# Performance work log

Measured on AMD Instinct MI355X. Metric: run time of the kernel, lower is better.

Reference implementation:

```python
import jax, jax.numpy as jnp
import numpy as np

NUM_GROUPS = 32
EPS = 1e-5


def _conv(x, w, b, pad):
    # x: [B,C,H,W], w: [O,I,kh,kw]
    y = jax.lax.conv_general_dilated(
        x, w, window_strides=(1, 1), padding=[(pad, pad), (pad, pad)],
        dimension_numbers=('NCHW', 'OIHW', 'NCHW'))
    return y + b[None, :, None, None]


def _group_norm(x, gamma, beta):
    B, C, H, W = x.shape
    g = x.reshape(B, NUM_GROUPS, C // NUM_GROUPS, H, W)
    mu = g.mean(axis=(2, 3, 4), keepdims=True)
    var = g.var(axis=(2, 3, 4), keepdims=True)
    g = (g - mu) * jax.lax.rsqrt(var + EPS)
    x = g.reshape(B, C, H, W)
    return x * gamma[None, :, None, None] + beta[None, :, None, None]


def setup_inputs() -> dict:
    key = jax.random.key(0)
    ks = jax.random.split(key, 8)
    B, C, H, W = 8, 384, 64, 64
    s1 = 1.0 / np.sqrt(C)          # 1x1 conv fan-in
    s3 = 1.0 / np.sqrt(C * 9)      # 3x3 conv fan-in
    return {
        'x': jax.random.normal(ks[0], (B, C, H, W), dtype=jnp.float32),
        'gamma': jnp.ones((C,), dtype=jnp.float32),
        'beta': jnp.zeros((C,), dtype=jnp.float32),
        'wq': jax.random.normal(ks[1], (C, C, 1, 1), dtype=jnp.float32) * s1,
        'bq': jnp.zeros((C,), dtype=jnp.float32),
        'wk': jax.random.normal(ks[2], (C, C, 3, 3), dtype=jnp.float32) * s3,
        'bk': jnp.zeros((C,), dtype=jnp.float32),
        'wv': jax.random.normal(ks[3], (C, C, 1, 1), dtype=jnp.float32) * s1,
        'bv': jnp.zeros((C,), dtype=jnp.float32),
        'wf': jax.random.normal(ks[4], (C, C, 1, 1), dtype=jnp.float32) * s1,
        'bf': jnp.zeros((C,), dtype=jnp.float32),
        'k': 512,
    }


def reference(x, gamma, beta, wq, bq, wk, bk, wv, bv, wf, bf, k):
    B, C, H, W = x.shape
    xn = _group_norm(x, gamma, beta)
    q = _conv(xn, wq, bq, 0)
    kk = _conv(xn, wk, bk, 1)
    v = _conv(xn, wv, bv, 0)
    # frequency-domain correlation: elementwise product of 2D spectra
    Fq = jnp.fft.fft2(q)
    Fk = jnp.fft.fft2(kk)
    A = jnp.fft.ifft2(Fq * Fk).real          # [B,C,H,W]
    # per-(batch,channel) spatial top-k sparsification
    A_flat = A.reshape(B, C, H * W)
    topv, _ = jax.lax.top_k(A_flat, k)
    thresh = topv[..., -1:]                   # k-th largest value
    masked = jnp.where(A_flat >= thresh, A_flat, -jnp.inf)
    Fw = jax.nn.softmax(masked, axis=-1).reshape(B, C, H, W)
    F4 = v * Fw                               # weighted values
    res = _conv(F4, wf, bf, 0)
    return xn * res
```

## Files before the change

kernel.cpp:

```cpp
#include <hip/hip_runtime.h>
#include <hip/hip_fp16.h>
#include <math.h>

#define CCH  384
#define BATCH 8
#define HWN  4096
#define NG   32
#define CPG  12
#define KSEL 512
#define FFTP 65

typedef short v8s  __attribute__((ext_vector_type(8)));
typedef float v16f __attribute__((ext_vector_type(16)));

#define MFMA_B16(A_,B_,C_) __builtin_amdgcn_mfma_f32_32x32x16_bf16((A_),(B_),(C_),0,0,0)

#define BARRIER_RAW() asm volatile("s_barrier" ::: "memory")

__device__ __forceinline__ void gl16(const unsigned short* g, unsigned short* l) {
  __builtin_amdgcn_global_load_lds(
      (const __attribute__((address_space(1))) unsigned int*)g,
      (__attribute__((address_space(3))) unsigned int*)l, 16, 0, 0);
}

__device__ __forceinline__ v8s as_v8s(uint4 u) {
  union { uint4 u4; v8s v; } c; c.u4 = u; return c.v;
}
__device__ __forceinline__ unsigned br6(unsigned i) {
  return ((i&1u)<<5)|((i&2u)<<3)|((i&4u)<<1)|((i&8u)>>1)|((i&16u)>>3)|((i&32u)>>5);
}
__device__ __forceinline__ unsigned f2key(float f) {
  unsigned u = __float_as_uint(f);
  return (u & 0x80000000u) ? ~u : (u | 0x80000000u);
}
__device__ __forceinline__ float wave_max(float v) {
#pragma unroll
  for (int o = 32; o > 0; o >>= 1) v = fmaxf(v, __shfl_down(v, o, 64));
  return v;
}
__device__ __forceinline__ float wave_sum(float v) {
#pragma unroll
  for (int o = 32; o > 0; o >>= 1) v += __shfl_down(v, o, 64);
  return v;
}
__device__ __forceinline__ unsigned short bf16_rne(float f) {
  unsigned u = __float_as_uint(f);
  return (unsigned short)((u + 0x7fffu + ((u >> 16) & 1u)) >> 16);
}
__device__ __forceinline__ float bf2f(unsigned short h) {
  return __uint_as_float(((unsigned)h) << 16);
}

__global__ __launch_bounds__(256) void stats_kernel(const float* __restrict__ x,
                                                    float2* __restrict__ gs,
                                                    unsigned short* __restrict__ zp) {
  int b = blockIdx.x >> 5, g = blockIdx.x & 31;
  if (blockIdx.x == 0 && threadIdx.x < 8) zp[threadIdx.x] = 0;
  size_t base = ((size_t)b * CCH + (size_t)g * CPG) * HWN;
  const float4* xp = (const float4*)(x + base);
  int tid = threadIdx.x;
  const int N4 = CPG * HWN / 4;
  float s = 0.f, ss = 0.f;
  for (int i = tid; i < N4; i += 256) {
    float4 v = xp[i];
    s  += (v.x + v.y) + (v.z + v.w);
    ss += (v.x*v.x + v.y*v.y) + (v.z*v.z + v.w*v.w);
  }
  s = wave_sum(s); ss = wave_sum(ss);
  __shared__ float sb[4], qb[4];
  if ((tid & 63) == 0) { sb[tid >> 6] = s; qb[tid >> 6] = ss; }
  __syncthreads();
  if (tid == 0) {
    float S = sb[0]+sb[1]+sb[2]+sb[3], Q = qb[0]+qb[1]+qb[2]+qb[3];
    float inv = 1.0f / (float)(CPG * HWN);
    float mu = S * inv;
    float var = Q * inv - mu * mu;
    gs[blockIdx.x] = make_float2(mu, rsqrtf(var + 1e-5f));
  }
}

__global__ __launch_bounds__(256) void pack_split_k(const float* __restrict__ w,
    unsigned short* __restrict__ hi, unsigned short* __restrict__ lo, int n) {
  int i = blockIdx.x * 256 + threadIdx.x;
  if (i >= n) return;
  float f = w[i];
  int m = i / 384, ci = i - m * 384;
  int kc = ci >> 4, tt = ci & 15;
  int mb = m >> 5, lm2 = m & 31;
  int l = ((tt >> 3) << 5) | lm2;
  int j = tt & 7;
  size_t o = (((size_t)kc * 12 + mb) << 9) + ((size_t)l << 3) + j;
  unsigned short h = bf16_rne(f);
  hi[o] = h;
  lo[o] = bf16_rne(f - bf2f(h));
}
__global__ __launch_bounds__(256) void pack9_k(const float* __restrict__ w,
    unsigned short* __restrict__ hi, unsigned short* __restrict__ lo) {
  int i = blockIdx.x * 256 + threadIdx.x;
  int r = blockIdx.y;
  float f = w[(size_t)i * 9 + r];
  int m = i / 384, ci = i - m * 384;
  int kc = ci >> 4, tt = ci & 15;
  int mb = m >> 5, lm2 = m & 31;
  int l = ((tt >> 3) << 5) | lm2;
  int j = tt & 7;
  size_t o = (((size_t)(r * 24 + kc) * 12 + mb) << 9) + ((size_t)l << 3) + j;
  unsigned short h = bf16_rne(f);
  hi[o] = h;
  lo[o] = bf16_rne(f - bf2f(h));
}

template<int FUSE, int SPLIT>
__global__ __launch_bounds__(256) void trans_kernel(const float* __restrict__ in,
    const float2* __restrict__ gs, const float* __restrict__ gamma,
    const float* __restrict__ beta,
    unsigned short* __restrict__ oh, unsigned short* __restrict__ ol) {
  __shared__ float ts[64][65];
  int tid = threadIdx.x;
  int b = blockIdx.z, c0 = blockIdx.y * 64, p0 = blockIdx.x * 64;
#pragma unroll
  for (int i = 0; i < 4; ++i) {
    int idx = tid + (i << 8);
    int row = idx >> 4, col = (idx & 15) << 2;
    float4 v = *(const float4*)&in[((size_t)b*CCH + c0 + row)*HWN + p0 + col];
    if (FUSE) {
      int c = c0 + row;
      float2 st = gs[(b << 5) + c / CPG];
      float a = gamma[c] * st.y, bb = beta[c] - st.x * a;
      v.x = v.x*a+bb; v.y = v.y*a+bb; v.z = v.z*a+bb; v.w = v.w*a+bb;
    }
    ts[row][col] = v.x; ts[row][col+1] = v.y; ts[row][col+2] = v.z; ts[row][col+3] = v.w;
  }
  __syncthreads();
#pragma unroll
  for (int i = 0; i < 2; ++i) {
    int idx = tid + (i << 8);
    int p = idx >> 3, cgp = (idx & 7) << 3;
    unsigned short h8[8] __attribute__((aligned(16)));
    unsigned short l8[8] __attribute__((aligned(16)));
#pragma unroll
    for (int j = 0; j < 8; ++j) {
      float f = ts[cgp + j][p];
      unsigned short hb = bf16_rne(f);
      h8[j] = hb;
      if (SPLIT) l8[j] = bf16_rne(f - bf2f(hb));
    }
    size_t o = ((size_t)b*HWN + p0 + p)*CCH + c0 + cgp;
    *(uint4*)&oh[o] = *(const uint4*)h8;
    if (SPLIT) *(uint4*)&ol[o] = *(const uint4*)l8;
  }
}

template<int TAPS, int OUT>
__global__ __launch_bounds__(256, 4) void mm_kernel(
    const unsigned short* __restrict__ Ahg, const unsigned short* __restrict__ Alg,
    const float* __restrict__ bias,
    const unsigned short* __restrict__ Bhg, const unsigned short* __restrict__ Blg,
    const unsigned short* __restrict__ xnTh, const unsigned short* __restrict__ xnTl,
    const unsigned short* __restrict__ zp,
    void* __restrict__ Yv) {
  __shared__ unsigned short Bh_s[2][4096], Bl_s[2][4096];
  int tid = threadIdx.x;
  int b = blockIdx.z, m0 = blockIdx.y * 128, n0 = blockIdx.x * 128;
  int y0 = blockIdx.x * 2;
  int lane = tid & 63, wm = tid >> 7, wn = (tid >> 6) & 1;
  int lm = lane & 31, lh = lane >> 5;
  int mbb = blockIdx.y * 4 + wm * 2;
  int laneoff = lane << 3;

  v16f acc[2][2];
#pragma unroll
  for (int t = 0; t < 2; ++t)
#pragma unroll
    for (int s = 0; s < 2; ++s)
#pragma unroll
      for (int g = 0; g < 16; ++g) acc[t][s][g] = 0.f;

  const int NS = TAPS * 12;
  uint4 rA0h_0, rA0l_0, rA1h_0, rA1l_0;
  uint4 rA0h_1, rA0l_1, rA1h_1, rA1l_1;

  auto stage = [&](int s) {
    int nxt = s & 1;
    int r  = (TAPS == 9) ? (s / 12) : 0;
    int c0 = (s - r * 12) * 32;
    int dy = (TAPS == 9) ? r / 3 - 1 : 0;
    int dx = (TAPS == 9) ? r % 3 - 1 : 0;
    int px = (tid >> 2) + dx;
    bool okx = (unsigned)px < 64u;
    int ch = c0 + (((tid & 3) ^ ((tid >> 3) & 3)) << 3);
    int lo = tid << 3;
#pragma unroll
    for (int c = 0; c < 2; ++c) {
      int py = y0 + dy + c;
      bool ok = okx && ((unsigned)py < 64u);
      size_t go = ok ? (((size_t)b * HWN + py * 64 + px) * CCH + ch) : 0;
      const unsigned short* gh = ok ? (Bhg + go) : zp;
      const unsigned short* gl = ok ? (Blg + go) : zp;
      gl16(gh, &Bh_s[nxt][lo + c * 2048]);
      gl16(gl, &Bl_s[nxt][lo + c * 2048]);
    }
  };
  auto loadA_h0 = [&](int s) {
    int fragcol;
    if (TAPS == 9) { int r = s / 12; fragcol = r * 24 + (s - r * 12) * 2; }
    else fragcol = s * 2;
    size_t off = (((size_t)fragcol * 12 + mbb) << 9) + laneoff;
    rA0h_0 = *(const uint4*)(Ahg + off);
    rA0l_0 = *(const uint4*)(Alg + off);
    rA1h_0 = *(const uint4*)(Ahg + off + 512);
    rA1l_0 = *(const uint4*)(Alg + off + 512);
  };
  auto loadA_h1 = [&](int s) {
    int fragcol;
    if (TAPS == 9) { int r = s / 12; fragcol = r * 24 + (s - r * 12) * 2 + 1; }
    else fragcol = s * 2 + 1;
    size_t off = (((size_t)fragcol * 12 + mbb) << 9) + laneoff;
    rA0h_1 = *(const uint4*)(Ahg + off);
    rA0l_1 = *(const uint4*)(Alg + off);
    rA1h_1 = *(const uint4*)(Ahg + off + 512);
    rA1l_1 = *(const uint4*)(Alg + off + 512);
  };
  auto ldB = [&](const unsigned short* base, int sb, int slot) -> v8s {
    int row = wn * 64 + sb * 32 + lm;
    int se = slot ^ ((row >> 1) & 3);
    return *(const v8s*)&base[row * 32 + (se << 3)];
  };

  stage(0);
  __builtin_amdgcn_sched_barrier(0);
  loadA_h0(0);
  __syncthreads();

  for (int s = 0; s < NS; ++s) {
    const unsigned short* Bhc = &Bh_s[s & 1][0];
    const unsigned short* Blc = &Bl_s[s & 1][0];
    if (s + 1 < NS) stage(s + 1);
    __builtin_amdgcn_sched_barrier(0);
    loadA_h1(s);
    {
      v8s b0h = ldB(Bhc, 0, lh),     b1h = ldB(Bhc, 1, lh);
      v8s b0l = ldB(Blc, 0, lh),     b1l = ldB(Blc, 1, lh);
      v8s a0h = as_v8s(rA0h_0), a0l = as_v8s(rA0l_0);
      v8s a1h = as_v8s(rA1h_0), a1l = as_v8s(rA1l_0);
      __builtin_amdgcn_s_setprio(1);
      acc[0][0] = MFMA_B16(a0h, b0h, acc[0][0]);
      acc[0][1] = MFMA_B16(a0h, b1h, acc[0][1]);
      acc[1][0] = MFMA_B16(a1h, b0h, acc[1][0]);
      acc[1][1] = MFMA_B16(a1h, b1h, acc[1][1]);
      acc[0][0] = MFMA_B16(a0h, b0l, acc[0][0]);
      acc[0][1] = MFMA_B16(a0h, b1l, acc[0][1]);
      acc[1][0] = MFMA_B16(a1h, b0l, acc[1][0]);
      acc[1][1] = MFMA_B16(a1h, b1l, acc[1][1]);
      acc[0][0] = MFMA_B16(a0l, b0h, acc[0][0]);
      acc[0][1] = MFMA_B16(a0l, b1h, acc[0][1]);
      acc[1][0] = MFMA_B16(a1l, b0h, acc[1][0]);
      acc[1][1] = MFMA_B16(a1l, b1h, acc[1][1]);
      __builtin_amdgcn_s_setprio(0);
    }
    if (s + 1 < NS) loadA_h0(s + 1);
    {
      v8s b0h = ldB(Bhc, 0, 2 + lh), b1h = ldB(Bhc, 1, 2 + lh);
      v8s b0l = ldB(Blc, 0, 2 + lh), b1l = ldB(Blc, 1, 2 + lh);
      v8s a0h = as_v8s(rA0h_1), a0l = as_v8s(rA0l_1);
      v8s a1h = as_v8s(rA1h_1), a1l = as_v8s(rA1l_1);
      __builtin_amdgcn_s_setprio(1);
      acc[0][0] = MFMA_B16(a0h, b0h, acc[0][0]);
      acc[0][1] = MFMA_B16(a0h, b1h, acc[0][1]);
      acc[1][0] = MFMA_B16(a1h, b0h, acc[1][0]);
      acc[1][1] = MFMA_B16(a1h, b1h, acc[1][1]);
      acc[0][0] = MFMA_B16(a0h, b0l, acc[0][0]);
      acc[0][1] = MFMA_B16(a0h, b1l, acc[0][1]);
      acc[1][0] = MFMA_B16(a1h, b0l, acc[1][0]);
      acc[1][1] = MFMA_B16(a1h, b1l, acc[1][1]);
      acc[0][0] = MFMA_B16(a0l, b0h, acc[0][0]);
      acc[0][1] = MFMA_B16(a0l, b1h, acc[0][1]);
      acc[1][0] = MFMA_B16(a1l, b0h, acc[1][0]);
      acc[1][1] = MFMA_B16(a1l, b1h, acc[1][1]);
      __builtin_amdgcn_s_setprio(0);
    }
    BARRIER_RAW();
  }
#pragma unroll
  for (int t = 0; t < 2; ++t) {
    int mb = m0 + wm * 64 + t * 32;
#pragma unroll
    for (int s = 0; s < 2; ++s) {
      int n = n0 + wn * 64 + s * 32 + lm;
#pragma unroll
      for (int g = 0; g < 16; ++g) {
        int m = mb + (g & 3) + ((g >> 2) << 3) + (lh << 2);
        float val = acc[t][s][g] + bias[m];
        size_t oidx = ((size_t)b * CCH + m) * HWN + n;
        if (OUT == 0) {
          ((float*)Yv)[oidx] = val;
        } else if (OUT == 1) {
          ((__half*)Yv)[oidx] = __float2half(val);
        } else {
          size_t tix = ((size_t)b * HWN + n) * CCH + m;
          float xnv = bf2f(xnTh[tix]) + bf2f(xnTl[tix]);
          ((float*)Yv)[oidx] = val * xnv;
        }
      }
    }
  }
}

__device__ __forceinline__ void fft4_pass(float* zr, float* zi,
    const float* twr, const float* twi, int tid, int axis, float ds) {
#pragma unroll
  for (int s = 0; s < 3; ++s) {
    const int h = 1 << (2 * s);
#pragma unroll
    for (int tt = 0; tt < 4; ++tt) {
      int t = tid + (tt << 8);
      int line = t >> 4, bf = t & 15;
      int j  = bf & (h - 1);
      int i0 = ((bf >> (2 * s)) << (2 * s + 2)) + j;
      int e1 = j << (5 - 2 * s);
      int e2 = j << (4 - 2 * s);
      float w1r = twr[e1], w1i = ds * twi[e1];
      float w2r = twr[e2], w2i = ds * twi[e2];
      int A0, st;
      if (axis == 0) { A0 = line * FFTP + i0; st = h; }
      else           { A0 = i0 * FFTP + line; st = h * FFTP; }
      int A1 = A0 + st, A2 = A1 + st, A3 = A2 + st;
      float x0r = zr[A0], x0i = zi[A0];
      float x1r = zr[A1], x1i = zi[A1];
      float x2r = zr[A2], x2i = zi[A2];
      float x3r = zr[A3], x3i = zi[A3];
      float t1r = x1r*w1r - x1i*w1i, t1i = x1r*w1i + x1i*w1r;
      float t3r = x3r*w1r - x3i*w1i, t3i = x3r*w1i + x3i*w1r;
      float u0r = x0r + t1r, u0i = x0i + t1i;
      float u1r = x0r - t1r, u1i = x0i - t1i;
      float u2r = x2r + t3r, u2i = x2i + t3i;
      float u3r = x2r - t3r, u3i = x2i - t3i;
      float c2r = u2r*w2r - u2i*w2i, c2i = u2r*w2i + u2i*w2r;
      float c3r = u3r*w2r - u3i*w2i, c3i = u3r*w2i + u3i*w2r;
      zr[A0] = u0r + c2r;      zi[A0] = u0i + c2i;
      zr[A2] = u0r - c2r;      zi[A2] = u0i - c2i;
      zr[A1] = u1r + ds*c3i;   zi[A1] = u1i - ds*c3r;
      zr[A3] = u1r - ds*c3i;   zi[A3] = u1i + ds*c3r;
    }
    __syncthreads();
  }
}

__global__ __launch_bounds__(256) void fft_topk_kernel(
    const float* q, const float* __restrict__ kkb,
    const __half* __restrict__ v, float* F4) {
  __shared__ float zr[64 * FFTP], zi[64 * FFTP];
  __shared__ float twr[32], twi[32];
  __shared__ unsigned hist[256];
  __shared__ unsigned su2[2];
  __shared__ unsigned wtot[4];
  __shared__ float sred[5];
  int tid = threadIdx.x;
  int lane = tid & 63, w = tid >> 6;
  size_t base = (size_t)blockIdx.x * HWN;
  for (int i = tid; i < HWN; i += 256) {
    int y = i >> 6, x = i & 63;
    int slot = br6(y) * FFTP + br6(x);
    zr[slot] = q[base + i];
    zi[slot] = kkb[base + i];
  }
  if (tid < 32) {
    float ang = (float)tid * 0.0981747704246810387f;
    twr[tid] = cosf(ang);
    twi[tid] = -sinf(ang);
  }
  __syncthreads();
  fft4_pass(zr, zi, twr, twi, tid, 0, 1.f);
  fft4_pass(zr, zi, twr, twi, tid, 1, 1.f);
  float prr[16], pir[16];
#pragma unroll
  for (int c = 0; c < 16; c++) {
    int i = tid + (c << 8);
    int ky = i >> 6, kx = i & 63;
    float sr = zr[ky * FFTP + kx], si = zi[ky * FFTP + kx];
    int kyn = (64 - ky) & 63, kxn = (64 - kx) & 63;
    float nr = zr[kyn * FFTP + kxn], ni = zi[kyn * FFTP + kxn];
    float fqr = 0.5f * (sr + nr), fqi = 0.5f * (si - ni);
    float fkr = 0.5f * (si + ni), fki = 0.5f * (nr - sr);
    prr[c] = fqr * fkr - fqi * fki;
    pir[c] = fqr * fki + fqi * fkr;
  }
  __syncthreads();
#pragma unroll
  for (int c = 0; c < 16; c++) {
    int i = tid + (c << 8);
    int ky = i >> 6, kx = i & 63;
    int slot = br6(ky) * FFTP + br6(kx);
    zr[slot] = prr[c];
    zi[slot] = pir[c];
  }
  __syncthreads();
  fft4_pass(zr, zi, twr, twi, tid, 0, -1.f);
  fft4_pass(zr, zi, twr, twi, tid, 1, -1.f);
  const float scale = 1.0f / 4096.0f;
  float a[16];
  unsigned key[16];
  float mx = -3.0e38f;
#pragma unroll
  for (int c = 0; c < 16; c++) {
    int i = tid + (c << 8);
    a[c] = zr[(i >> 6) * FFTP + (i & 63)] * scale;
    key[c] = f2key(a[c]);
    mx = fmaxf(mx, a[c]);
  }
  mx = wave_max(mx);
  if (lane == 0) sred[w] = mx;
  __syncthreads();
  if (tid == 0) sred[4] = fmaxf(fmaxf(sred[0], sred[1]), fmaxf(sred[2], sred[3]));
  __syncthreads();
  float am = sred[4];
  unsigned prefix = 0; int kr = KSEL;
  for (int pass = 0; pass < 4; pass++) {
    int shift = 24 - (pass << 3);
    hist[tid] = 0;
    __syncthreads();
#pragma unroll
    for (int c = 0; c < 16; c++) {
      unsigned u = key[c];
      if (((u ^ prefix) >> shift) <= 0xFFu)
        atomicAdd(&hist[(u >> shift) & 255u], 1u);
    }
    __syncthreads();
    unsigned xv = hist[tid];
#pragma unroll
    for (int o = 1; o < 64; o <<= 1) {
      unsigned t2 = __shfl_down(xv, o, 64);
      if (lane + o < 64) xv += t2;
    }
    if (lane == 0) wtot[w] = xv;
    __syncthreads();
    for (int ww = w + 1; ww < 4; ++ww) xv += wtot[ww];
    hist[tid] = xv;
    __syncthreads();
    unsigned sv = xv;
    unsigned svn = (tid < 255) ? hist[tid + 1] : 0u;
    if (sv >= (unsigned)kr && svn < (unsigned)kr) { su2[0] = (unsigned)tid; su2[1] = svn; }
    __syncthreads();
    prefix |= su2[0] << shift;
    kr -= (int)su2[1];
  }
  unsigned thr = prefix;
  float lsum = 0.f;
#pragma unroll
  for (int c = 0; c < 16; c++)
    if (key[c] >= thr) lsum += expf(a[c] - am);
  lsum = wave_sum(lsum);
  if (lane == 0) sred[w] = lsum;
  __syncthreads();
  if (tid == 0) sred[4] = 1.0f / (sred[0] + sred[1] + sred[2] + sred[3]);
  __syncthreads();
  float inv = sred[4];
#pragma unroll
  for (int c = 0; c < 16; c++) {
    int i = tid + (c << 8);
    float wgt = (key[c] >= thr) ? expf(a[c] - am) * inv : 0.f;
    F4[base + i] = __half2float(v[base + i]) * wgt;
  }
}

extern "C" void kernel_launch(void* const* d_in, const int* in_sizes, int n_in,
                              void* d_out, int out_size, void* d_ws, size_t ws_size,
                              hipStream_t stream) {
  const float* x     = (const float*)d_in[0];
  const float* gamma = (const float*)d_in[1];
  const float* beta  = (const float*)d_in[2];
  const float* wq    = (const float*)d_in[3];
  const float* bq    = (const float*)d_in[4];
  const float* wk    = (const float*)d_in[5];
  const float* bk    = (const float*)d_in[6];
  const float* wv    = (const float*)d_in[7];
  const float* bv    = (const float*)d_in[8];
  const float* wf    = (const float*)d_in[9];
  const float* bf    = (const float*)d_in[10];

  const size_t NEL = (size_t)BATCH * CCH * HWN;
  const size_t WSZ = (size_t)CCH * CCH;

  unsigned short* xnTh = (unsigned short*)d_ws;
  unsigned short* xnTl = xnTh + NEL;
  float*  qC  = (float*)(xnTl + NEL);
  float*  kD  = qC + NEL;
  __half* vE  = (__half*)(kD + NEL);
  unsigned short* W = (unsigned short*)(vE + NEL);
  unsigned short* Wqh = W;
  unsigned short* Wql = Wqh + WSZ;
  unsigned short* Wvh = Wql + WSZ;
  unsigned short* Wvl = Wvh + WSZ;
  unsigned short* Wfh = Wvl + WSZ;
  unsigned short* Wfl = Wfh + WSZ;
  unsigned short* Wkh = Wfl + WSZ;
  unsigned short* Wkl = Wkh + 9 * WSZ;
  float2* gs = (float2*)(Wkl + 9 * WSZ);
  unsigned short* zp = (unsigned short*)(gs + BATCH * NG);
  unsigned short* F4Th = (unsigned short*)kD;
  unsigned short* F4Tl = F4Th + NEL;

  pack_split_k<<<dim3(576), dim3(256), 0, stream>>>(wq, Wqh, Wql, (int)WSZ);
  pack_split_k<<<dim3(576), dim3(256), 0, stream>>>(wv, Wvh, Wvl, (int)WSZ);
  pack_split_k<<<dim3(576), dim3(256), 0, stream>>>(wf, Wfh, Wfl, (int)WSZ);
  pack9_k<<<dim3(576, 9), dim3(256), 0, stream>>>(wk, Wkh, Wkl);
  stats_kernel<<<dim3(BATCH * NG), dim3(256), 0, stream>>>(x, gs, zp);
  trans_kernel<1, 1><<<dim3(64, 6, BATCH), dim3(256), 0, stream>>>(
      x, gs, gamma, beta, xnTh, xnTl);

  dim3 gm(32, 3, BATCH);
  mm_kernel<1, 0><<<gm, dim3(256), 0, stream>>>(Wqh, Wql, bq, xnTh, xnTl,
                                                nullptr, nullptr, zp, qC);
  mm_kernel<9, 0><<<gm, dim3(256), 0, stream>>>(Wkh, Wkl, bk, xnTh, xnTl,
                                                nullptr, nullptr, zp, kD);
  mm_kernel<1, 1><<<gm, dim3(256), 0, stream>>>(Wvh, Wvl, bv, xnTh, xnTl,
                                                nullptr, nullptr, zp, vE);

  fft_topk_kernel<<<dim3(BATCH * CCH), dim3(256), 0, stream>>>(qC, kD, vE, qC);

  trans_kernel<0, 1><<<dim3(64, 6, BATCH), dim3(256), 0, stream>>>(
      qC, nullptr, nullptr, nullptr, F4Th, F4Tl);

  mm_kernel<1, 2><<<gm, dim3(256), 0, stream>>>(Wfh, Wfl, bf, F4Th, F4Tl,
                                                xnTh, xnTl, zp, d_out);
}
```

Baseline: 730.6 us.

## Triple-buffer LDS B tiles with two-stage-ahead prefetch in conv GEMM

Moves the MFMA conv GEMM from double to triple buffering of the shared-memory B tiles. Global-to-LDS copies are now issued two k-steps ahead, A fragments are prefetched a full step ahead into alternating register sets, and the loop uses explicit vmcnt waits with barriers around each MFMA group. Occupancy drops from 4 to 3 blocks per CU, and there are more barriers and registers per step. This trades occupancy for deeper latency hiding of global loads. Correctness relies on the hand-counted vmcnt values and on NS being even.

Result: faster. 687.6 us (-5.9%).

```diff
diff --git a/kernel.cpp b/kernel.cpp
--- a/kernel.cpp
+++ b/kernel.cpp
@@ -151,15 +151,20 @@
   }
 }
 
+struct AFrag {
+  uint4 a0h_0, a0l_0, a1h_0, a1l_0;
+  uint4 a0h_1, a0l_1, a1h_1, a1l_1;
+};
+
 template<int TAPS, int OUT>
-__global__ __launch_bounds__(256, 4) void mm_kernel(
+__global__ __launch_bounds__(256, 3) void mm_kernel(
     const unsigned short* __restrict__ Ahg, const unsigned short* __restrict__ Alg,
     const float* __restrict__ bias,
     const unsigned short* __restrict__ Bhg, const unsigned short* __restrict__ Blg,
     const unsigned short* __restrict__ xnTh, const unsigned short* __restrict__ xnTl,
     const unsigned short* __restrict__ zp,
     void* __restrict__ Yv) {
-  __shared__ unsigned short Bh_s[2][4096], Bl_s[2][4096];
+  __shared__ unsigned short Bh_s[3][4096], Bl_s[3][4096];
   int tid = threadIdx.x;
   int b = blockIdx.z, m0 = blockIdx.y * 128, n0 = blockIdx.x * 128;
   int y0 = blockIdx.x * 2;
@@ -177,11 +182,8 @@
       for (int g = 0; g < 16; ++g) acc[t][s][g] = 0.f;
 
   const int NS = TAPS * 12;
-  uint4 rA0h_0, rA0l_0, rA1h_0, rA1l_0;
-  uint4 rA0h_1, rA0l_1, rA1h_1, rA1l_1;
-
-  auto stage = [&](int s) {
-    int nxt = s & 1;
+
+  auto stage = [&](int s, int dst) {
     int r  = (TAPS == 9) ? (s / 12) : 0;
     int c0 = (s - r * 12) * 32;
     int dy = (TAPS == 9) ? r / 3 - 1 : 0;
@@ -197,90 +199,96 @@
       size_t go = ok ? (((size_t)b * HWN + py * 64 + px) * CCH + ch) : 0;
       const unsigned short* gh = ok ? (Bhg + go) : zp;
       const unsigned short* gl = ok ? (Blg + go) : zp;
-      gl16(gh, &Bh_s[nxt][lo + c * 2048]);
-      gl16(gl, &Bl_s[nxt][lo + c * 2048]);
+      gl16(gh, &Bh_s[dst][lo + c * 2048]);
+      gl16(gl, &Bl_s[dst][lo + c * 2048]);
     }
   };
-  auto loadA_h0 = [&](int s) {
+  auto loadA_h0 = [&](int s, AFrag& F) {
     int fragcol;
     if (TAPS == 9) { int r = s / 12; fragcol = r * 24 + (s - r * 12) * 2; }
     else fragcol = s * 2;
     size_t off = (((size_t)fragcol * 12 + mbb) << 9) + laneoff;
-    rA0h_0 = *(const uint4*)(Ahg + off);
-    rA0l_0 = *(const uint4*)(Alg + off);
-    rA1h_0 = *(const uint4*)(Ahg + off + 512);
-    rA1l_0 = *(const uint4*)(Alg + off + 512);
+    F.a0h_0 = *(const uint4*)(Ahg + off);
+    F.a0l_0 = *(const uint4*)(Alg + off);
+    F.a1h_0 = *(const uint4*)(Ahg + off + 512);
+    F.a1l_0 = *(const uint4*)(Alg + off + 512);
   };
-  auto loadA_h1 = [&](int s) {
+  auto loadA_h1 = [&](int s, AFrag& F) {
     int fragcol;
     if (TAPS == 9) { int r = s / 12; fragcol = r * 24 + (s - r * 12) * 2 + 1; }
     else fragcol = s * 2 + 1;
     size_t off = (((size_t)fragcol * 12 + mbb) << 9) + laneoff;
-    rA0h_1 = *(const uint4*)(Ahg + off);
-    rA0l_1 = *(const uint4*)(Alg + off);
-    rA1h_1 = *(const uint4*)(Ahg + off + 512);
-    rA1l_1 = *(const uint4*)(Alg + off + 512);
+    F.a0h_1 = *(const uint4*)(Ahg + off);
+    F.a0l_1 = *(const uint4*)(Alg + off);
+    F.a1h_1 = *(const uint4*)(Ahg + off + 512);
+    F.a1l_1 = *(const uint4*)(Alg + off + 512);
   };
   auto ldB = [&](const unsigned short* base, int sb, int slot) -> v8s {
     int row = wn * 64 + sb * 32 + lm;
     int se = slot ^ ((row >> 1) & 3);
     return *(const v8s*)&base[row * 32 + (se << 3)];
   };
-
-  stage(0);
-  __builtin_amdgcn_sched_barrier(0);
-  loadA_h0(0);
-  __syncthreads();
-
-  for (int s = 0; s < NS; ++s) {
-    const unsigned short* Bhc = &Bh_s[s & 1][0];
-    const unsigned short* Blc = &Bl_s[s & 1][0];
-    if (s + 1 < NS) stage(s + 1);
+  auto mfma12 = [&](v8s a0h, v8s a0l, v8s a1h, v8s a1l,
+                    v8s b0h, v8s b0l, v8s b1h, v8s b1l) {
+    __builtin_amdgcn_s_setprio(1);
+    acc[0][0] = MFMA_B16(a0h, b0h, acc[0][0]);
+    acc[0][1] = MFMA_B16(a0h, b1h, acc[0][1]);
+    acc[1][0] = MFMA_B16(a1h, b0h, acc[1][0]);
+    acc[1][1] = MFMA_B16(a1h, b1h, acc[1][1]);
+    acc[0][0] = MFMA_B16(a0h, b0l, acc[0][0]);
+    acc[0][1] = MFMA_B16(a0h, b1l, acc[0][1]);
+    acc[1][0] = MFMA_B16(a1h, b0l, acc[1][0]);
+    acc[1][1] = MFMA_B16(a1h, b1l, acc[1][1]);
+    acc[0][0] = MFMA_B16(a0l, b0h, acc[0][0]);
+    acc[0][1] = MFMA_B16(a0l, b1h, acc[0][1]);
+    acc[1][0] = MFMA_B16(a1l, b0h, acc[1][0]);
+    acc[1][1] = MFMA_B16(a1l, b1h, acc[1][1]);
+    __builtin_amdgcn_s_setprio(0);
+  };
+
+  auto doStep = [&](int s, int cur, int wb, AFrag& Ac, AFrag& An) {
+    const unsigned short* Bhc = &Bh_s[cur][0];
+    const unsigned short* Blc = &Bl_s[cur][0];
+    v8s b0h = ldB(Bhc, 0, lh),     b1h = ldB(Bhc, 1, lh);
+    v8s b0l = ldB(Blc, 0, lh),     b1l = ldB(Blc, 1, lh);
+    if (s + 1 < NS) loadA_h0(s + 1, An);
+    if (s + 2 < NS) stage(s + 2, wb);
+    BARRIER_RAW();
+    mfma12(as_v8s(Ac.a0h_0), as_v8s(Ac.a0l_0), as_v8s(Ac.a1h_0), as_v8s(Ac.a1l_0),
+           b0h, b0l, b1h, b1l);
+    BARRIER_RAW();
+    v8s c0h = ldB(Bhc, 0, 2 + lh), c1h = ldB(Bhc, 1, 2 + lh);
+    v8s c0l = ldB(Blc, 0, 2 + lh), c1l = ldB(Blc, 1, 2 + lh);
+    if (s + 1 < NS) loadA_h1(s + 1, An);
     __builtin_amdgcn_sched_barrier(0);
-    loadA_h1(s);
-    {
-      v8s b0h = ldB(Bhc, 0, lh),     b1h = ldB(Bhc, 1, lh);
-      v8s b0l = ldB(Blc, 0, lh),     b1l = ldB(Blc, 1, lh);
-      v8s a0h = as_v8s(rA0h_0), a0l = as_v8s(rA0l_0);
-      v8s a1h = as_v8s(rA1h_0), a1l = as_v8s(rA1l_0);
-      __builtin_amdgcn_s_setprio(1);
-      acc[0][0] = MFMA_B16(a0h, b0h, acc[0][0]);
-      acc[0][1] = MFMA_B16(a0h, b1h, acc[0][1]);
-      acc[1][0] = MFMA_B16(a1h, b0h, acc[1][0]);
-      acc[1][1] = MFMA_B16(a1h, b1h, acc[1][1]);
-      acc[0][0] = MFMA_B16(a0h, b0l, acc[0][0]);
-      acc[0][1] = MFMA_B16(a0h, b1l, acc[0][1]);
-      acc[1][0] = MFMA_B16(a1h, b0l, acc[1][0]);
-      acc[1][1] = MFMA_B16(a1h, b1l, acc[1][1]);
-      acc[0][0] = MFMA_B16(a0l, b0h, acc[0][0]);
-      acc[0][1] = MFMA_B16(a0l, b1h, acc[0][1]);
-      acc[1][0] = MFMA_B16(a1l, b0h, acc[1][0]);
-      acc[1][1] = MFMA_B16(a1l, b1h, acc[1][1]);
-      __builtin_amdgcn_s_setprio(0);
-    }
-    if (s + 1 < NS) loadA_h0(s + 1);
-    {
-      v8s b0h = ldB(Bhc, 0, 2 + lh), b1h = ldB(Bhc, 1, 2 + lh);
-      v8s b0l = ldB(Blc, 0, 2 + lh), b1l = ldB(Blc, 1, 2 + lh);
-      v8s a0h = as_v8s(rA0h_1), a0l = as_v8s(rA0l_1);
-      v8s a1h = as_v8s(rA1h_1), a1l = as_v8s(rA1l_1);
-      __builtin_amdgcn_s_setprio(1);
-      acc[0][0] = MFMA_B16(a0h, b0h, acc[0][0]);
-      acc[0][1] = MFMA_B16(a0h, b1h, acc[0][1]);
-      acc[1][0] = MFMA_B16(a1h, b0h, acc[1][0]);
-      acc[1][1] = MFMA_B16(a1h, b1h, acc[1][1]);
-      acc[0][0] = MFMA_B16(a0h, b0l, acc[0][0]);
-      acc[0][1] = MFMA_B16(a0h, b1l, acc[0][1]);
-      acc[1][0] = MFMA_B16(a1h, b0l, acc[1][0]);
-      acc[1][1] = MFMA_B16(a1h, b1l, acc[1][1]);
-      acc[0][0] = MFMA_B16(a0l, b0h, acc[0][0]);
-      acc[0][1] = MFMA_B16(a0l, b1h, acc[0][1]);
-      acc[1][0] = MFMA_B16(a1l, b0h, acc[1][0]);
-      acc[1][1] = MFMA_B16(a1l, b1h, acc[1][1]);
-      __builtin_amdgcn_s_setprio(0);
-    }
+    if (s + 2 < NS) {
+      asm volatile("s_waitcnt vmcnt(16)" ::: "memory");
+    } else if (s + 1 < NS) {
+      asm volatile("s_waitcnt vmcnt(12)" ::: "memory");
+    }
+    __builtin_amdgcn_sched_barrier(0);
     BARRIER_RAW();
-  }
+    mfma12(as_v8s(Ac.a0h_1), as_v8s(Ac.a0l_1), as_v8s(Ac.a1h_1), as_v8s(Ac.a1l_1),
+           c0h, c0l, c1h, c1l);
+    BARRIER_RAW();
+  };
+
+  AFrag Aa, Ab;
+  stage(0, 0);
+  stage(1, 1);
+  loadA_h0(0, Aa); loadA_h1(0, Aa);
+  __syncthreads();
+
+  int cur = 0;
+  for (int s = 0; s < NS; s += 2) {
+    int w0 = (cur >= 1) ? cur - 1 : 2;
+    doStep(s, cur, w0, Aa, Ab);
+    int c1 = (cur + 1 >= 3) ? 0 : cur + 1;
+    int w1 = (c1 >= 1) ? c1 - 1 : 2;
+    doStep(s + 1, c1, w1, Ab, Aa);
+    cur = (c1 + 1 >= 3) ? 0 : c1 + 1;
+  }
+
 #pragma unroll
   for (int t = 0; t < 2; ++t) {
     int mb = m0 + wm * 64 + t * 32;
```
